# Kernel optimization log

Hardware: AMD Instinct MI355X
Metric: run time of the kernel (lower is better)

## Reference

```python
import jax, jax.numpy as jnp
import numpy as np


def setup_inputs() -> dict:
    key = jax.random.key(0)
    ks = jax.random.split(key, 8)
    nf, nloc, nnei, ng2 = 1, 1024, 128, 32
    nd, nh = 32, 4
    g2 = jax.random.normal(ks[0], (nf, nloc, nnei, ng2), jnp.float32)
    h2 = jax.random.normal(ks[1], (nf, nloc, nnei, 3), jnp.float32)
    sw = jax.random.uniform(ks[2], (nf, nloc, nnei), jnp.float32)
    nlist_mask = jax.random.randint(ks[3], (nf, nloc, nnei), 0, 2).astype(jnp.int32)
    w_qk = jax.random.normal(ks[4], (ng2, nd * 2 * nh), jnp.float32) / np.sqrt(ng2)
    w_v = jax.random.normal(ks[5], (ng2, ng2 * nh), jnp.float32) / np.sqrt(ng2)
    w_head = jax.random.normal(ks[6], (ng2 * nh, ng2), jnp.float32) / np.sqrt(ng2 * nh)
    b_head = jnp.zeros((ng2,), jnp.float32)
    w_eqhead = jax.random.normal(ks[7], (nh, 1), jnp.float32) / np.sqrt(nh)
    return dict(g2=g2, h2=h2, sw=sw, w_qk=w_qk, w_v=w_v, w_head=w_head,
                b_head=b_head, w_eqhead=w_eqhead, nlist_mask=nlist_mask)


def reference(g2, h2, sw, w_qk, w_v, w_head, b_head, w_eqhead, nlist_mask):
    ATTNW_SHIFT = 20.0
    nf, nloc, nnei, ng2 = g2.shape
    nh = w_eqhead.shape[0]
    nd = w_qk.shape[1] // (2 * nh)
    mask = nlist_mask.astype(bool)

    # --- Atten2Map: build gated, smoothed multi-head attention A[b,i,h,q,k] ---
    qk = (g2 @ w_qk).reshape(nf, nloc, nnei, nd, 2 * nh)
    qk = jnp.transpose(qk, (0, 1, 4, 2, 3))            # (b, i, 2nh, nnei, nd)
    q, k = qk[:, :, :nh], qk[:, :, nh:]
    A = jnp.einsum('bihqd,bihkd->bihqk', q, k) / jnp.sqrt(jnp.float32(nd))
    h2ht = jnp.einsum('biqc,bikc->biqk', h2, h2)       # h2 @ h2^T (gate, pre-scale)
    A = A * h2ht[:, :, None]                            # has_gate=True
    swq = sw[:, :, None, :, None]
    swk = sw[:, :, None, None, :]
    A = (A + ATTNW_SHIFT) * swq * swk - ATTNW_SHIFT     # smooth shift
    A = jax.nn.softmax(A, axis=-1)
    A = jnp.where(mask[:, :, None, None, :], A, 0.0)   # attnw_mask (keys)
    A = jnp.where(mask[:, :, None, :, None], A, 0.0)   # attnw_mask_c (queries)
    A = A * swq * swk
    A = A * (h2ht / jnp.sqrt(jnp.float32(3.0)))[:, :, None]  # * h2h2t/sqrt(3)

    # --- Atten2MultiHeadApply: invariant g2 update ---
    g2v = (g2 @ w_v).reshape(nf, nloc, nnei, ng2, nh)
    out_g = jnp.einsum('bihqk,bikgh->biqgh', A, g2v).reshape(nf, nloc, nnei, ng2 * nh)
    g2_out = out_g @ w_head + b_head

    # --- Atten2EquiVarApply: equivariant h2 update ---
    out_h = jnp.einsum('bihqk,bikc->biqch', A, h2)      # (b, i, nnei, 3, nh)
    h2_out = (out_h @ w_eqhead)[..., 0]                 # (b, i, nnei, 3)
    return g2_out, h2_out
```

## Files before the change

### kernel.cpp

```cpp
#include <hip/hip_runtime.h>


typedef __bf16 v8bf __attribute__((ext_vector_type(8)));
typedef float  v4f  __attribute__((ext_vector_type(4)));
typedef unsigned u32x2 __attribute__((ext_vector_type(2)));
typedef unsigned u32x4 __attribute__((ext_vector_type(4)));

__device__ __forceinline__ float b2f(unsigned short b) {
    union { unsigned u; float f; } x; x.u = ((unsigned)b) << 16; return x.f;
}
__device__ __forceinline__ unsigned short fb(float f) {
    return __builtin_bit_cast(unsigned short, (__bf16)f);
}
struct HL { unsigned short hi, lo; };
__device__ __forceinline__ HL splitbf(float f) {
    HL r; r.hi = fb(f); r.lo = fb(f - b2f(r.hi)); return r;
}
__device__ __forceinline__ unsigned pk2(unsigned short lo, unsigned short hi) {
    return ((unsigned)hi << 16) | (unsigned)lo;
}
__device__ __forceinline__ unsigned cvt2(float a, float b) {
    return pk2(fb(a), fb(b));
}
__device__ __forceinline__ void sp2(float a, float b, unsigned& hi, unsigned& lo) {
    __bf16 ah = (__bf16)a, bh = (__bf16)b;
    hi = pk2(__builtin_bit_cast(unsigned short, ah), __builtin_bit_cast(unsigned short, bh));
    lo = cvt2(a - (float)ah, b - (float)bh);
}
__device__ __forceinline__ v8bf mkv8(unsigned a, unsigned b, unsigned c, unsigned d) {
    u32x4 x = {a, b, c, d};
    return __builtin_bit_cast(v8bf, x);
}
__device__ __forceinline__ float hwe(const float* h2s, int kn,
                                     float hq0, float hq1, float hq2) {
    const v4f hk = *(const v4f*)(h2s + kn * 4);
    return fmaf(hq2, hk[2], fmaf(hq1, hk[1], hq0 * hk[0]));
}

#define MF(a,b,c) __builtin_amdgcn_mfma_f32_16x16x32_bf16((a),(b),(c),0,0,0)
#define FENCE() asm volatile("" ::: "memory")

#if __has_builtin(__builtin_amdgcn_exp2f)
#define EXP2(x) __builtin_amdgcn_exp2f(x)
#else
#define EXP2(x) __expf((x) * 0.6931471805599453f)
#endif

#define MSH (-28.853900817779268f)

#define G2H 0
#define G2L 4096
#define G2T 8192
#define NQH 12544
#define NQL 16640
#define H2T 20736
#define PQ  21280
#define SM_U16 25376

#define RPERM(C) ((((C) >> 2) & 1) * 16 + (((C) >> 3) << 2) + ((C) & 3))
#define KEY(R) ((((R) & 3) ^ (((R) >> 3) & 3)) << 3)

#define CC_(a,b) a##b
#define CC(a,b) CC_(a,b)

#define LD8(NM, IDX) \
    HL CC(NM,0) = splitbf(IDX(0)), CC(NM,1) = splitbf(IDX(1)), \
       CC(NM,2) = splitbf(IDX(2)), CC(NM,3) = splitbf(IDX(3)), \
       CC(NM,4) = splitbf(IDX(4)), CC(NM,5) = splitbf(IDX(5)), \
       CC(NM,6) = splitbf(IDX(6)), CC(NM,7) = splitbf(IDX(7));
#define HI8(NM) mkv8(pk2(CC(NM,0).hi, CC(NM,1).hi), pk2(CC(NM,2).hi, CC(NM,3).hi), \
                     pk2(CC(NM,4).hi, CC(NM,5).hi), pk2(CC(NM,6).hi, CC(NM,7).hi))
#define LO8(NM) mkv8(pk2(CC(NM,0).lo, CC(NM,1).lo), pk2(CC(NM,2).lo, CC(NM,3).lo), \
                     pk2(CC(NM,4).lo, CC(NM,5).lo), pk2(CC(NM,6).lo, CC(NM,7).lo))

__global__ __launch_bounds__(512, 3) void repformer_kernel(
    const float* __restrict__ g2, const float* __restrict__ h2,
    const float* __restrict__ sw, const float* __restrict__ wqk,
    const float* __restrict__ wv, const float* __restrict__ wh,
    const float* __restrict__ bh, const float* __restrict__ weq,
    const int*   __restrict__ nmask, float* __restrict__ out)
{
    __shared__ __align__(16) unsigned short sm[SM_U16];
    __shared__ __align__(16) float smf[772];
    float* h2s = smf;
    float* sws = smf + 512;
    float* es  = smf + 640;
    float* wqs = smf + 768;

    const int t    = threadIdx.x;
    const int i    = blockIdx.x;
    const int lane = t & 63;
    const int w8   = t >> 6;
    const int quad = lane >> 4;
    const int n16  = lane & 15;
    const int h    = w8 & 3;
    const int mt   = w8 >> 2;

    {
        const float4* src = (const float4*)(g2 + (size_t)i * 4096);
        #pragma unroll
        for (int j = 0; j < 2; j++) {
            int idx = j * 512 + t;
            float4 v = src[idx];
            HL a0 = splitbf(v.x), a1 = splitbf(v.y), a2 = splitbf(v.z), a3 = splitbf(v.w);
            int k = idx >> 3, c0 = (idx & 7) * 4;
            int swz = k * 32 + (c0 ^ KEY(k));
            *(u32x2*)(sm + G2H + swz) = (u32x2){pk2(a0.hi, a1.hi), pk2(a2.hi, a3.hi)};
            *(u32x2*)(sm + G2L + swz) = (u32x2){pk2(a0.lo, a1.lo), pk2(a2.lo, a3.lo)};
            sm[G2T + RPERM(c0 + 0) * 136 + k] = a0.hi;
            sm[G2T + RPERM(c0 + 1) * 136 + k] = a1.hi;
            sm[G2T + RPERM(c0 + 2) * 136 + k] = a2.hi;
            sm[G2T + RPERM(c0 + 3) * 136 + k] = a3.hi;
        }
    }
    if (t < 384) {
        float f = h2[(size_t)i * 384 + t];
        int k = t / 3, c = t - k * 3;
        h2s[k * 4 + c] = f;
        sm[H2T + c * 136 + k] = fb(f);
    }
    if (t < 128) {
        sm[H2T + 3 * 136 + t] = 0;
        float s = sw[i * 128 + t];
        sws[t] = s;
        es[t]  = (nmask[i * 128 + t] != 0) ? s : 0.0f;
    }
    if (t < 4) wqs[t] = weq[t];

#define WKI(J) wqk[(mt * 16 + n16) * 256 + (quad * 8 + (J)) * 8 + 4 + h]
#define WVI(J) wv[(mt * 16 + n16) * 128 + (quad * 8 + (J)) * 4 + h]
#define WQI(J) wqk[(nt * 16 + n16) * 256 + (quad * 8 + (J)) * 8 + h]
#define WHI(J) wh[((quad * 8 + (J)) * 4 + h) * 32 + nt * 16 + n16]
    {
        LD8(ak, WKI)
        LD8(av, WVI)
        const v8bf akh = HI8(ak), akl = LO8(ak);
        const v8bf avh = HI8(av), avl = LO8(av);
        FENCE();
        #pragma unroll 1
        for (int nt = 0; nt < 2; nt++) {
            LD8(bq, WQI)
            LD8(bw, WHI)
            const v8bf bqh = HI8(bq), bql = LO8(bq);
            const v8bf bhh = HI8(bw), bhl = LO8(bw);
            FENCE();
            const v4f z = {0.f, 0.f, 0.f, 0.f};
            v4f c1 = MF(akh, bqh, MF(akl, bqh, MF(akh, bql, z)));
            #pragma unroll
            for (int r = 0; r < 4; r++) {
                HL s1 = splitbf(c1[r]);
                int x    = mt * 16 + quad * 4 + r;
                int rowp = RPERM(x);
                int addr = h * 1024 + rowp * 32 + ((nt * 16 + n16) ^ KEY(rowp));
                sm[NQH + addr] = s1.hi; sm[NQL + addr] = s1.lo;
            }
            v4f c2 = MF(avh, bhh, MF(avl, bhh, MF(avh, bhl, z)));
            #pragma unroll
            for (int r = 0; r < 4; r++) {
                int o  = nt * 16 + n16;
                int cw = mt * 16 + quad * 4 + r;
                sm[PQ + h * 1024 + o * 32 + (cw ^ KEY(o))] = fb(c2[r]);
            }
            FENCE();
        }
    }
    __syncthreads();

    {
        int kcol = t & 127;
        int cb = (t >> 7) * 8;
        float ek = es[kcol];
        #pragma unroll
        for (int c = 0; c < 8; c++) {
            int idx = G2T + (cb + c) * 136 + kcol;
            sm[idx] = fb(b2f(sm[idx]) * ek);
        }
        if (t < 128) {
            #pragma unroll
            for (int c = 0; c < 3; c++) {
                int idx = H2T + c * 136 + t;
                sm[idx] = fb(b2f(sm[idx]) * es[t]);
            }
        }
    }
    __syncthreads();

    const int hr = (n16 < 3) ? n16 : 3;
    float* outg = out;
    float* outh = out + 4194304;
    const float bias0 = bh[n16];
    const float bias1 = bh[16 + n16];
    const int qo0 = (quad * 8) ^ KEY(n16);
    const int qo1 = (quad * 8) ^ KEY(16 + n16);
    const int rowbase = ((n16 >> 2) << 3) + (n16 & 3);
    const int qoK = (quad * 8) ^ KEY(rowbase);
    const unsigned short* g2t0 = sm + G2T + n16 * 136;
    const unsigned short* g2t1 = sm + G2T + (16 + n16) * 136;
    const unsigned short* h2tp = sm + H2T + hr * 136;

#define KSSTEP(KS, HWA, HWB) { \
    const int rowA = (KS) * 32 + rowbase; \
    const v8bf ah0 = *(const v8bf*)(sm + G2H + rowA * 32 + qoK); \
    const v8bf al0 = *(const v8bf*)(sm + G2L + rowA * 32 + qoK); \
    const v8bf ah1 = *(const v8bf*)(sm + G2H + (rowA + 4) * 32 + qoK); \
    const v8bf al1 = *(const v8bf*)(sm + G2L + (rowA + 4) * 32 + qoK); \
    const v4f st0 = MF(ah0, ql, MF(al0, qh, MF(ah0, qh, vz))); \
    const v4f st1 = MF(ah1, ql, MF(al1, qh, MF(ah1, qh, vz))); \
    const v4f swkA = *(const v4f*)(sws + (KS) * 32 + quad * 8); \
    const v4f swkB = *(const v4f*)(sws + (KS) * 32 + quad * 8 + 4); \
    const float p0 = EXP2(fmaf(fmaf(st0[0], (HWA)[0], swq20E), swkA[0], MSH)); \
    const float p1 = EXP2(fmaf(fmaf(st0[1], (HWA)[1], swq20E), swkA[1], MSH)); \
    const float p2 = EXP2(fmaf(fmaf(st0[2], (HWA)[2], swq20E), swkA[2], MSH)); \
    const float p3 = EXP2(fmaf(fmaf(st0[3], (HWA)[3], swq20E), swkA[3], MSH)); \
    const float p4 = EXP2(fmaf(fmaf(st1[0], (HWB)[0], swq20E), swkB[0], MSH)); \
    const float p5 = EXP2(fmaf(fmaf(st1[1], (HWB)[1], swq20E), swkB[1], MSH)); \
    const float p6 = EXP2(fmaf(fmaf(st1[2], (HWB)[2], swq20E), swkB[2], MSH)); \
    const float p7 = EXP2(fmaf(fmaf(st1[3], (HWB)[3], swq20E), swkB[3], MSH)); \
    sum += ((p0 + p1) + (p2 + p3)) + ((p4 + p5) + (p6 + p7)); \
    const v8bf pv = mkv8(cvt2(p0 * (HWA)[0], p1 * (HWA)[1]), \
                         cvt2(p2 * (HWA)[2], p3 * (HWA)[3]), \
                         cvt2(p4 * (HWB)[0], p5 * (HWB)[1]), \
                         cvt2(p6 * (HWB)[2], p7 * (HWB)[3])); \
    T0  = MF(*(const v8bf*)(g2t0 + (KS) * 32 + quad * 8), pv, T0); \
    T1  = MF(*(const v8bf*)(g2t1 + (KS) * 32 + quad * 8), pv, T1); \
    ohl = MF(*(const v8bf*)(h2tp + (KS) * 32 + quad * 8), pv, ohl); \
}

    {
        const int s = w8;
        const int q = s * 16 + n16;
        const int qoq = (quad * 8) ^ KEY(q);
        const v8bf gfh = *(const v8bf*)(sm + G2H + q * 32 + qoq);
        const v8bf gfl = *(const v8bf*)(sm + G2L + q * 32 + qoq);
        const float swq    = sws[q];
        const float mq     = (es[q] != 0.0f) ? 1.0f : 0.0f;
        const float swq20E = swq * 28.853900817779268f;
        const float kq     = 0.17677669529663687f * 1.4426950408889634f * swq;
        const float hq0 = h2s[q * 4 + 0] * kq;
        const float hq1 = h2s[q * 4 + 1] * kq;
        const float hq2 = h2s[q * 4 + 2] * kq;
#define HW4(T8) (v4f){ hwe(h2s, ((T8) >> 1) * 32 + quad * 8 + ((T8) & 1) * 4 + 0, hq0, hq1, hq2), \
                       hwe(h2s, ((T8) >> 1) * 32 + quad * 8 + ((T8) & 1) * 4 + 1, hq0, hq1, hq2), \
                       hwe(h2s, ((T8) >> 1) * 32 + quad * 8 + ((T8) & 1) * 4 + 2, hq0, hq1, hq2), \
                       hwe(h2s, ((T8) >> 1) * 32 + quad * 8 + ((T8) & 1) * 4 + 3, hq0, hq1, hq2) }
        const v4f hw0 = HW4(0), hw1 = HW4(1), hw2 = HW4(2), hw3 = HW4(3);
        const v4f hw4 = HW4(4), hw5 = HW4(5), hw6 = HW4(6), hw7 = HW4(7);
        v4f og0 = {0.f, 0.f, 0.f, 0.f}, og1 = og0, ohacc = og0;
        FENCE();

        #pragma unroll 1
        for (int hd = 0; hd < 4; hd++) {
            const v4f vz = {0.f, 0.f, 0.f, 0.f};
            const unsigned short* nqh = sm + NQH + hd * 1024;
            const unsigned short* nql = sm + NQL + hd * 1024;
            const v8bf nh0 = *(const v8bf*)(nqh + n16 * 32 + qo0);
            const v8bf nl0 = *(const v8bf*)(nql + n16 * 32 + qo0);
            const v8bf nh1 = *(const v8bf*)(nqh + (16 + n16) * 32 + qo1);
            const v8bf nl1 = *(const v8bf*)(nql + (16 + n16) * 32 + qo1);
            v4f c0t = MF(nh0, gfl, MF(nl0, gfh, MF(nh0, gfh, vz)));
            v4f c1t = MF(nh1, gfl, MF(nl1, gfh, MF(nh1, gfh, vz)));
            unsigned qh0, qh1, qh2, qh3, ql0, ql1, ql2, ql3;
            sp2(c0t[0], c0t[1], qh0, ql0);
            sp2(c0t[2], c0t[3], qh1, ql1);
            sp2(c1t[0], c1t[1], qh2, ql2);
            sp2(c1t[2], c1t[3], qh3, ql3);
            const v8bf qh = mkv8(qh0, qh1, qh2, qh3);
            const v8bf ql = mkv8(ql0, ql1, ql2, ql3);
            v4f T0 = vz, T1 = vz, ohl = vz;
            float sum = 0.f;
            KSSTEP(0, hw0, hw1)
            KSSTEP(1, hw2, hw3)
            FENCE();
            KSSTEP(2, hw4, hw5)
            KSSTEP(3, hw6, hw7)
            sum += __shfl_xor(sum, 16, 64);
            sum += __shfl_xor(sum, 32, 64);
            const float scale = mq * 2.2638092f * __builtin_amdgcn_rcpf(sum);
            const v8bf ta = mkv8(cvt2(scale * T0[0], scale * T0[1]),
                                 cvt2(scale * T0[2], scale * T0[3]),
                                 cvt2(scale * T1[0], scale * T1[1]),
                                 cvt2(scale * T1[2], scale * T1[3]));
            const unsigned short* wp = sm + PQ + hd * 1024;
            og0 = MF(ta, *(const v8bf*)(wp + n16 * 32 + qo0), og0);
            og1 = MF(ta, *(const v8bf*)(wp + (16 + n16) * 32 + qo1), og1);
            const float ws = wqs[hd] * scale;
            ohacc[0] = fmaf(ws, ohl[0], ohacc[0]);
            ohacc[1] = fmaf(ws, ohl[1], ohacc[1]);
            ohacc[2] = fmaf(ws, ohl[2], ohacc[2]);
            ohacc[3] = fmaf(ws, ohl[3], ohacc[3]);
            FENCE();
        }

        const int qg = i * 128 + s * 16;
        #pragma unroll
        for (int r = 0; r < 4; r++) {
            outg[(size_t)(qg + quad * 4 + r) * 32 + n16]      = og0[r] + bias0;
            outg[(size_t)(qg + quad * 4 + r) * 32 + 16 + n16] = og1[r] + bias1;
        }
        if (quad == 0) {
            #pragma unroll
            for (int r = 0; r < 3; r++)
                outh[(size_t)(qg + n16) * 3 + r] = ohacc[r];
        }
    }
}

extern "C" void kernel_launch(void* const* d_in, const int* in_sizes, int n_in,
                              void* d_out, int out_size, void* d_ws, size_t ws_size,
                              hipStream_t stream) {
    const float* g2  = (const float*)d_in[0];
    const float* h2  = (const float*)d_in[1];
    const float* sw  = (const float*)d_in[2];
    const float* wqk = (const float*)d_in[3];
    const float* wv  = (const float*)d_in[4];
    const float* wh  = (const float*)d_in[5];
    const float* bh  = (const float*)d_in[6];
    const float* weq = (const float*)d_in[7];
    const int*   nm  = (const int*)d_in[8];
    int nloc = in_sizes[0] / (128 * 32);
    repformer_kernel<<<nloc, 512, 0, stream>>>(g2, h2, sw, wqk, wv, wh, bh, weq, nm, (float*)d_out);
}
```

Baseline: 131.0 us.

## Precompute folded weight products in a separate kernel and read them from global memory

The per-block weight folding (Wq·Wk^T and Wv·Whead products, split into bf16 hi/lo) moves into a single-block pre-kernel that writes them to workspace. The main kernel then reads these operands from global/L2 instead of LDS. The edge-weight scaling of the transposed g2/h2 tiles is now applied at load time, which removes a shared-memory pass and one barrier. LDS use drops from about 50KB to 26KB and launch bounds rise to 4 blocks/CU, at the cost of an extra launch and global loads inside the head loop.

```diff
diff --git a/kernel.cpp b/kernel.cpp
--- a/kernel.cpp
+++ b/kernel.cpp
@@ -48,14 +48,15 @@
 
 #define MSH (-28.853900817779268f)
 
+#define NQHo 0
+#define NQLo 4096
+#define PQo  8192
+
 #define G2H 0
 #define G2L 4096
 #define G2T 8192
-#define NQH 12544
-#define NQL 16640
-#define H2T 20736
-#define PQ  21280
-#define SM_U16 25376
+#define H2T 12544
+#define SM_U16 13088
 
 #define RPERM(C) ((((C) >> 2) & 1) * 16 + (((C) >> 3) << 2) + ((C) & 3))
 #define KEY(R) ((((R) & 3) ^ (((R) >> 3) & 3)) << 3)
@@ -73,12 +74,61 @@
 #define LO8(NM) mkv8(pk2(CC(NM,0).lo, CC(NM,1).lo), pk2(CC(NM,2).lo, CC(NM,3).lo), \
                      pk2(CC(NM,4).lo, CC(NM,5).lo), pk2(CC(NM,6).lo, CC(NM,7).lo))
 
-__global__ __launch_bounds__(512, 3) void repformer_kernel(
+#define WKI(J) wqk[(mt * 16 + n16) * 256 + (quad * 8 + (J)) * 8 + 4 + h]
+#define WVI(J) wv[(mt * 16 + n16) * 128 + (quad * 8 + (J)) * 4 + h]
+#define WQI(J) wqk[(nt * 16 + n16) * 256 + (quad * 8 + (J)) * 8 + h]
+#define WHI(J) wh[((quad * 8 + (J)) * 4 + h) * 32 + nt * 16 + n16]
+
+__global__ __launch_bounds__(512) void fold_kernel(
+    const float* __restrict__ wqk, const float* __restrict__ wv,
+    const float* __restrict__ wh, unsigned short* __restrict__ wsu)
+{
+    const int t    = threadIdx.x;
+    const int lane = t & 63;
+    const int w8   = t >> 6;
+    const int quad = lane >> 4;
+    const int n16  = lane & 15;
+    const int h    = w8 & 3;
+    const int mt   = w8 >> 2;
+
+    LD8(ak, WKI)
+    LD8(av, WVI)
+    const v8bf akh = HI8(ak), akl = LO8(ak);
+    const v8bf avh = HI8(av), avl = LO8(av);
+    FENCE();
+    #pragma unroll 1
+    for (int nt = 0; nt < 2; nt++) {
+        LD8(bq, WQI)
+        LD8(bw, WHI)
+        const v8bf bqh = HI8(bq), bql = LO8(bq);
+        const v8bf bhh = HI8(bw), bhl = LO8(bw);
+        FENCE();
+        const v4f z = {0.f, 0.f, 0.f, 0.f};
+        v4f c1 = MF(akh, bqh, MF(akl, bqh, MF(akh, bql, z)));
+        #pragma unroll
+        for (int r = 0; r < 4; r++) {
+            HL s1 = splitbf(c1[r]);
+            int x    = mt * 16 + quad * 4 + r;
+            int rowp = RPERM(x);
+            int addr = h * 1024 + rowp * 32 + ((nt * 16 + n16) ^ KEY(rowp));
+            wsu[NQHo + addr] = s1.hi; wsu[NQLo + addr] = s1.lo;
+        }
+        v4f c2 = MF(avh, bhh, MF(avl, bhh, MF(avh, bhl, z)));
+        #pragma unroll
+        for (int r = 0; r < 4; r++) {
+            int o  = nt * 16 + n16;
+            int cw = mt * 16 + quad * 4 + r;
+            wsu[PQo + h * 1024 + o * 32 + (cw ^ KEY(o))] = fb(c2[r]);
+        }
+        FENCE();
+    }
+}
+
+__global__ __launch_bounds__(512, 4) void repformer_kernel(
     const float* __restrict__ g2, const float* __restrict__ h2,
-    const float* __restrict__ sw, const float* __restrict__ wqk,
-    const float* __restrict__ wv, const float* __restrict__ wh,
-    const float* __restrict__ bh, const float* __restrict__ weq,
-    const int*   __restrict__ nmask, float* __restrict__ out)
+    const float* __restrict__ sw, const float* __restrict__ bh,
+    const float* __restrict__ weq, const int* __restrict__ nmask,
+    const unsigned short* __restrict__ wsu, float* __restrict__ out)
 {
     __shared__ __align__(16) unsigned short sm[SM_U16];
     __shared__ __align__(16) float smf[772];
@@ -93,8 +143,6 @@
     const int w8   = t >> 6;
     const int quad = lane >> 4;
     const int n16  = lane & 15;
-    const int h    = w8 & 3;
-    const int mt   = w8 >> 2;
 
     {
         const float4* src = (const float4*)(g2 + (size_t)i * 4096);
@@ -107,17 +155,20 @@
             int swz = k * 32 + (c0 ^ KEY(k));
             *(u32x2*)(sm + G2H + swz) = (u32x2){pk2(a0.hi, a1.hi), pk2(a2.hi, a3.hi)};
             *(u32x2*)(sm + G2L + swz) = (u32x2){pk2(a0.lo, a1.lo), pk2(a2.lo, a3.lo)};
-            sm[G2T + RPERM(c0 + 0) * 136 + k] = a0.hi;
-            sm[G2T + RPERM(c0 + 1) * 136 + k] = a1.hi;
-            sm[G2T + RPERM(c0 + 2) * 136 + k] = a2.hi;
-            sm[G2T + RPERM(c0 + 3) * 136 + k] = a3.hi;
+            float ek = (nmask[i * 128 + k] != 0) ? sw[i * 128 + k] : 0.0f;
+            sm[G2T + RPERM(c0 + 0) * 136 + k] = fb(b2f(a0.hi) * ek);
+            sm[G2T + RPERM(c0 + 1) * 136 + k] = fb(b2f(a1.hi) * ek);
+            sm[G2T + RPERM(c0 + 2) * 136 + k] = fb(b2f(a2.hi) * ek);
+            sm[G2T + RPERM(c0 + 3) * 136 + k] = fb(b2f(a3.hi) * ek);
         }
     }
     if (t < 384) {
         float f = h2[(size_t)i * 384 + t];
         int k = t / 3, c = t - k * 3;
         h2s[k * 4 + c] = f;
-        sm[H2T + c * 136 + k] = fb(f);
+        float ek = (nmask[i * 128 + k] != 0) ? sw[i * 128 + k] : 0.0f;
+        unsigned short us = fb(f);
+        sm[H2T + c * 136 + k] = fb(b2f(us) * ek);
     }
     if (t < 128) {
         sm[H2T + 3 * 136 + t] = 0;
@@ -126,63 +177,6 @@
         es[t]  = (nmask[i * 128 + t] != 0) ? s : 0.0f;
     }
     if (t < 4) wqs[t] = weq[t];
-
-#define WKI(J) wqk[(mt * 16 + n16) * 256 + (quad * 8 + (J)) * 8 + 4 + h]
-#define WVI(J) wv[(mt * 16 + n16) * 128 + (quad * 8 + (J)) * 4 + h]
-#define WQI(J) wqk[(nt * 16 + n16) * 256 + (quad * 8 + (J)) * 8 + h]
-#define WHI(J) wh[((quad * 8 + (J)) * 4 + h) * 32 + nt * 16 + n16]
-    {
-        LD8(ak, WKI)
-        LD8(av, WVI)
-        const v8bf akh = HI8(ak), akl = LO8(ak);
-        const v8bf avh = HI8(av), avl = LO8(av);
-        FENCE();
-        #pragma unroll 1
-        for (int nt = 0; nt < 2; nt++) {
-            LD8(bq, WQI)
-            LD8(bw, WHI)
-            const v8bf bqh = HI8(bq), bql = LO8(bq);
-            const v8bf bhh = HI8(bw), bhl = LO8(bw);
-            FENCE();
-            const v4f z = {0.f, 0.f, 0.f, 0.f};
-            v4f c1 = MF(akh, bqh, MF(akl, bqh, MF(akh, bql, z)));
-            #pragma unroll
-            for (int r = 0; r < 4; r++) {
-                HL s1 = splitbf(c1[r]);
-                int x    = mt * 16 + quad * 4 + r;
-                int rowp = RPERM(x);
-                int addr = h * 1024 + rowp * 32 + ((nt * 16 + n16) ^ KEY(rowp));
-                sm[NQH + addr] = s1.hi; sm[NQL + addr] = s1.lo;
-            }
-            v4f c2 = MF(avh, bhh, MF(avl, bhh, MF(avh, bhl, z)));
-            #pragma unroll
-            for (int r = 0; r < 4; r++) {
-                int o  = nt * 16 + n16;
-                int cw = mt * 16 + quad * 4 + r;
-                sm[PQ + h * 1024 + o * 32 + (cw ^ KEY(o))] = fb(c2[r]);
-            }
-            FENCE();
-        }
-    }
-    __syncthreads();
-
-    {
-        int kcol = t & 127;
-        int cb = (t >> 7) * 8;
-        float ek = es[kcol];
-        #pragma unroll
-        for (int c = 0; c < 8; c++) {
-            int idx = G2T + (cb + c) * 136 + kcol;
-            sm[idx] = fb(b2f(sm[idx]) * ek);
-        }
-        if (t < 128) {
-            #pragma unroll
-            for (int c = 0; c < 3; c++) {
-                int idx = H2T + c * 136 + t;
-                sm[idx] = fb(b2f(sm[idx]) * es[t]);
-            }
-        }
-    }
     __syncthreads();
 
     const int hr = (n16 < 3) ? n16 : 3;
@@ -251,8 +245,8 @@
         #pragma unroll 1
         for (int hd = 0; hd < 4; hd++) {
             const v4f vz = {0.f, 0.f, 0.f, 0.f};
-            const unsigned short* nqh = sm + NQH + hd * 1024;
-            const unsigned short* nql = sm + NQL + hd * 1024;
+            const unsigned short* nqh = wsu + NQHo + hd * 1024;
+            const unsigned short* nql = wsu + NQLo + hd * 1024;
             const v8bf nh0 = *(const v8bf*)(nqh + n16 * 32 + qo0);
             const v8bf nl0 = *(const v8bf*)(nql + n16 * 32 + qo0);
             const v8bf nh1 = *(const v8bf*)(nqh + (16 + n16) * 32 + qo1);
@@ -280,7 +274,7 @@
                                  cvt2(scale * T0[2], scale * T0[3]),
                                  cvt2(scale * T1[0], scale * T1[1]),
                                  cvt2(scale * T1[2], scale * T1[3]));
-            const unsigned short* wp = sm + PQ + hd * 1024;
+            const unsigned short* wp = wsu + PQo + hd * 1024;
             og0 = MF(ta, *(const v8bf*)(wp + n16 * 32 + qo0), og0);
             og1 = MF(ta, *(const v8bf*)(wp + (16 + n16) * 32 + qo1), og1);
             const float ws = wqs[hd] * scale;
@@ -317,6 +311,8 @@
     const float* bh  = (const float*)d_in[6];
     const float* weq = (const float*)d_in[7];
     const int*   nm  = (const int*)d_in[8];
+    unsigned short* wsu = (unsigned short*)d_ws;
     int nloc = in_sizes[0] / (128 * 32);
-    repformer_kernel<<<nloc, 512, 0, stream>>>(g2, h2, sw, wqk, wv, wh, bh, weq, nm, (float*)d_out);
-}
+    fold_kernel<<<1, 512, 0, stream>>>(wqk, wv, wh, wsu);
+    repformer_kernel<<<nloc, 512, 0, stream>>>(g2, h2, sw, bh, weq, nm, wsu, (float*)d_out);
+}
```

Result: faster. 127.2 us (-3.0%).
